# Optimization experiments

Measured on AMD Instinct MI355X. Metric: run time of the kernel, lower is better.

Reference implementation:

```python
import jax, jax.numpy as jnp
import numpy as np

B, C, L, K = 64, 2, 131072, 4


def setup_inputs() -> dict:
    key = jax.random.key(0)
    k1, k2, k3, k4 = jax.random.split(key, 4)
    x = jax.random.normal(k1, (B, C, L), dtype=jnp.float32)
    Bs = 0.5 * jax.random.normal(k2, (B, C, K, 3), dtype=jnp.float32)
    # Build stable denominators: complex-conjugate poles r*exp(+-j*theta), r < 0.95
    # a(z) = 1 - 2 r cos(theta) z^-1 + r^2 z^-2  -> guaranteed-stable IIR cascade.
    r = jax.random.uniform(k3, (B, C, K), minval=0.1, maxval=0.95)
    theta = jax.random.uniform(k4, (B, C, K), minval=0.05, maxval=np.pi - 0.05)
    a1 = -2.0 * r * jnp.cos(theta)
    a2 = r * r
    As = jnp.stack([jnp.ones_like(a1), a1, a2], axis=-1).astype(jnp.float32)
    return {"input_signal": x, "Bs": Bs, "As": As}


def _biquad_cascade(x, b, a):
    # x: [N, L]; b, a: [N, K, 3] with a already normalized (a0 == 1).
    # Serial cascade of K biquads, each in direct form II transposed:
    #   y[n]  = b0*u[n] + s1
    #   s1'   = b1*u[n] - a1*y[n] + s2
    #   s2'   = b2*u[n] - a2*y[n]
    # Exactly the linear recurrence the ssm/lfilter backends compute.
    nK = b.shape[1]
    b0, b1, b2 = b[..., 0], b[..., 1], b[..., 2]  # each [N, K]
    a1, a2 = a[..., 1], a[..., 2]

    def step(carry, xt):
        s1, s2 = carry  # each [N, K]
        u = xt  # [N]
        s1n, s2n = [], []
        for k in range(nK):  # small fixed cascade depth, unrolled
            y = b0[:, k] * u + s1[:, k]
            s1n.append(b1[:, k] * u - a1[:, k] * y + s2[:, k])
            s2n.append(b2[:, k] * u - a2[:, k] * y)
            u = y
        return (jnp.stack(s1n, axis=1), jnp.stack(s2n, axis=1)), u

    N = x.shape[0]
    init = (jnp.zeros((N, nK), x.dtype), jnp.zeros((N, nK), x.dtype))
    _, ys = jax.lax.scan(step, init, x.T)  # scan over time: ys [L, N]
    return ys.T


def reference(input_signal, Bs, As):
    b, c, audio_len = input_signal.shape
    assert Bs.shape[-1] == As.shape[-1] == 3
    # channel broadcasting as in _process_ssm
    if c == 1 and Bs.shape[1] > 1:
        input_signal = jnp.broadcast_to(input_signal, (b, Bs.shape[1], audio_len))
        c = Bs.shape[1]
    elif Bs.shape[1] == 1 and c > 1:
        Bs = jnp.broadcast_to(Bs, (b, c) + Bs.shape[2:])
        As = jnp.broadcast_to(As, (b, c) + As.shape[2:])
    a0 = As[..., :1]
    Bn = (Bs / a0).reshape(b * c, -1, 3)
    An = (As / a0).reshape(b * c, -1, 3)
    x = input_signal.reshape(b * c, audio_len)
    y = _biquad_cascade(x, Bn, An)
    return y.reshape(b, c, audio_len)
```

## Files before the change

kernel.cpp:

```cpp
#include <hip/hip_runtime.h>
#include <math.h>


#define SS   64
#define WMAX 384
#define WMIN 64
#define TT   32
#define TPB  256
#define LSTR 33
#define KB   4
#define NL   8
#define HALO 6
#define DSTR 9

typedef float vf4 __attribute__((ext_vector_type(4)));

__global__ void iir_prep2_kernel(const float* __restrict__ Bs,
                                 const float* __restrict__ As, int rows,
                                 int* __restrict__ nwrow,
                                 float* __restrict__ nmat)
{
    __shared__ float mat[4][3][64];
    const int grp  = threadIdx.x >> 6;
    const int lane = threadIdx.x & 63;
    const int row  = blockIdx.x * 4 + grp;
    const bool act = (row < rows);

    float b0[KB], b1[KB], b2[KB], na1[KB], na2[KB];
    if (act) {
        const float* Bp = Bs + (size_t)row * KB * 3;
        const float* Ap = As + (size_t)row * KB * 3;
#pragma unroll
        for (int k = 0; k < KB; ++k) {
            float inv = 1.0f / Ap[3 * k];
            b0[k]  =  Bp[3 * k]     * inv;
            b1[k]  =  Bp[3 * k + 1] * inv;
            b2[k]  =  Bp[3 * k + 2] * inv;
            na1[k] = -Ap[3 * k + 1] * inv;
            na2[k] = -Ap[3 * k + 2] * inv;
        }
    }

    float* cur = &mat[grp][0][0];
    float* nxt = &mat[grp][1][0];
    float* n1  = &mat[grp][2][0];

    if (act && lane < 8) {
        float s[8];
#pragma unroll
        for (int i = 0; i < 8; ++i) s[i] = (i == lane) ? 1.0f : 0.0f;
        float u = 0.0f;
#pragma unroll
        for (int k = 0; k < KB; ++k) {
            float y  = fmaf(b0[k], u, s[2 * k]);
            float t1 = fmaf(na1[k], y, fmaf(b1[k], u, s[2 * k + 1]));
            float t2 = fmaf(na2[k], y, b2[k] * u);
            s[2 * k] = t1; s[2 * k + 1] = t2; u = y;
        }
#pragma unroll
        for (int i = 0; i < 8; ++i) cur[i * 8 + lane] = s[i];
    }
    __syncthreads();

    const int i8 = lane >> 3, j8 = lane & 7;

    for (int t = 0; t < 6; ++t) {
        float acc = 0.0f;
        if (act) {
#pragma unroll
            for (int m = 0; m < 8; ++m)
                acc = fmaf(cur[i8 * 8 + m], cur[m * 8 + j8], acc);
            nxt[lane] = acc;
        }
        __syncthreads();
        float* t0 = cur; cur = nxt; nxt = t0;
    }

    if (act) {
        float v = cur[lane];
        n1[lane] = v;
        nmat[(size_t)row * 320 + lane] = v;
    }
    __syncthreads();

    for (int m = 2; m <= 5; ++m) {
        float acc = 0.0f;
        if (act) {
#pragma unroll
            for (int q = 0; q < 8; ++q)
                acc = fmaf(cur[i8 * 8 + q], n1[q * 8 + j8], acc);
            nxt[lane] = acc;
            nmat[(size_t)row * 320 + (m - 1) * 64 + lane] = acc;
        }
        __syncthreads();
        float* t0 = cur; cur = nxt; nxt = t0;
    }

    if (act && lane == 0) {
        const float* Ap = As + (size_t)row * KB * 3;
        float r2max = 0.0f;
#pragma unroll
        for (int k = 0; k < KB; ++k) {
            float a0 = Ap[3 * k];
            float a2 = Ap[3 * k + 2] / a0;
            r2max = fmaxf(r2max, a2);
        }
        float rmax = fminf(fmaxf(sqrtf(fmaxf(r2max, 0.f)), 0.20f), 0.955f);
        float Wf = 25.6f / (-logf(rmax));
        int W = ((int)ceilf(Wf) + TT - 1) & ~(TT - 1);
        W = min(max(W, WMIN), WMAX);
        nwrow[row] = (W + SS - 1) / SS;
    }
}

__global__ __launch_bounds__(TPB, 4) void iir_state_kernel(
    const float* __restrict__ x, const float* __restrict__ Bs,
    const float* __restrict__ As, int L, float* __restrict__ dstate)
{
    __shared__ float lds[TPB * LSTR];
    const int tid = threadIdx.x;
    const int cpr = L / SS;
    const int bpr = cpr / TPB;
    const int row = blockIdx.x / bpr;
    const int chunk0 = (blockIdx.x % bpr) * TPB;

    float b0[KB], b1[KB], b2[KB], na1[KB], na2[KB];
    const float* Bp = Bs + (size_t)row * KB * 3;
    const float* Ap = As + (size_t)row * KB * 3;
#pragma unroll
    for (int k = 0; k < KB; ++k) {
        float inv = 1.0f / Ap[3 * k];
        b0[k]  =  Bp[3 * k]     * inv;
        b1[k]  =  Bp[3 * k + 1] * inv;
        b2[k]  =  Bp[3 * k + 2] * inv;
        na1[k] = -Ap[3 * k + 1] * inv;
        na2[k] = -Ap[3 * k + 2] * inv;
    }

    float s1[KB] = {0.f, 0.f, 0.f, 0.f};
    float s2[KB] = {0.f, 0.f, 0.f, 0.f};

    const float* xrow = x + (size_t)row * L;
    float* myrow = lds + tid * LSTR;

    const int tq = tid >> 3;
    const int p4 = (tid & 7) << 2;
    int off[NL], ldsoff[NL];
#pragma unroll
    for (int l = 0; l < NL; ++l) {
        int j = l * 32 + tq;
        off[l]    = (chunk0 + j) * SS + p4;
        ldsoff[l] = j * LSTR + p4;
    }

    float4 rn[NL];
#pragma unroll
    for (int l = 0; l < NL; ++l)
        rn[l] = *reinterpret_cast<const float4*>(xrow + off[l]);

#pragma unroll
    for (int it = 0; it < SS / TT; ++it) {
        __syncthreads();
#pragma unroll
        for (int l = 0; l < NL; ++l) {
            float* d = lds + ldsoff[l];
            d[0] = rn[l].x; d[1] = rn[l].y; d[2] = rn[l].z; d[3] = rn[l].w;
        }
        if (it + 1 < SS / TT) {
            const int base = (it + 1) * TT;
#pragma unroll
            for (int l = 0; l < NL; ++l)
                rn[l] = *reinterpret_cast<const float4*>(xrow + off[l] + base);
        }
        __syncthreads();

#pragma unroll
        for (int p = 0; p < TT; ++p) {
            float u = myrow[p];
#pragma unroll
            for (int k = 0; k < KB; ++k) {
                float yv = fmaf(b0[k], u, s1[k]);
                s1[k] = fmaf(na1[k], yv, fmaf(b1[k], u, s2[k]));
                s2[k] = fmaf(na2[k], yv, b2[k] * u);
                u = yv;
            }
        }
    }

    float* dp = dstate + ((size_t)row * cpr + chunk0 + tid) * 8;
    float4 d0 = make_float4(s1[0], s2[0], s1[1], s2[1]);
    float4 d1 = make_float4(s1[2], s2[2], s1[3], s2[3]);
    *reinterpret_cast<float4*>(dp)     = d0;
    *reinterpret_cast<float4*>(dp + 4) = d1;
}

__global__ __launch_bounds__(TPB, 4) void iir_out_kernel(
    const float* __restrict__ x, const float* __restrict__ Bs,
    const float* __restrict__ As, float* __restrict__ out, int L,
    const float* __restrict__ dstate, const float* __restrict__ nmat,
    const int* __restrict__ nwrow)
{
    __shared__ float lds[TPB * LSTR];
    const int tid = threadIdx.x;
    const int cpr = L / SS;
    const int bpr = cpr / TPB;
    const int row = blockIdx.x / bpr;
    const int chunk0 = (blockIdx.x % bpr) * TPB;
    const int nW = nwrow[row];

    float b0[KB], b1[KB], b2[KB], na1[KB], na2[KB];
    const float* Bp = Bs + (size_t)row * KB * 3;
    const float* Ap = As + (size_t)row * KB * 3;
#pragma unroll
    for (int k = 0; k < KB; ++k) {
        float inv = 1.0f / Ap[3 * k];
        b0[k]  =  Bp[3 * k]     * inv;
        b1[k]  =  Bp[3 * k + 1] * inv;
        b2[k]  =  Bp[3 * k + 2] * inv;
        na1[k] = -Ap[3 * k + 1] * inv;
        na2[k] = -Ap[3 * k + 2] * inv;
    }

    const float* xrow = x   + (size_t)row * L;
    float*       orow = out + (size_t)row * L;
    float*       myrow = lds + tid * LSTR;

    const int tq = tid >> 3;
    const int p4 = (tid & 7) << 2;
    int off[NL], ldsoff[NL];
#pragma unroll
    for (int l = 0; l < NL; ++l) {
        int j = l * 32 + tq;
        off[l]    = (chunk0 + j) * SS + p4;
        ldsoff[l] = j * LSTR + p4;
    }

    float4 rn[NL];
#pragma unroll
    for (int l = 0; l < NL; ++l)
        rn[l] = *reinterpret_cast<const float4*>(xrow + off[l]);

    float* dl = lds;
    float* nl = lds + (TPB + HALO) * DSTR;
    const float* dbase = dstate + ((size_t)row * cpr + chunk0 - HALO) * 8;
    for (int e = tid; e < (TPB + HALO) * 8; e += TPB) {
        int c  = e >> 3;
        int gi = chunk0 - HALO + c;
        float v = 0.0f;
        if (gi >= 0) v = dbase[e];
        dl[c * DSTR + (e & 7)] = v;
    }
    for (int e = tid; e < 320; e += TPB) nl[e] = nmat[(size_t)row * 320 + e];
    __syncthreads();

    float p[8];
#pragma unroll
    for (int i = 0; i < 8; ++i) p[i] = dl[(tid + HALO - 1) * DSTR + i];
#pragma unroll 1
    for (int m = 2; m <= nW; ++m) {
        const float* M  = nl + (m - 2) * 64;
        const float* dd = dl + (tid + HALO - m) * DSTR;
        float din[8];
#pragma unroll
        for (int q = 0; q < 8; ++q) din[q] = dd[q];
#pragma unroll
        for (int i = 0; i < 8; ++i) {
            float a = p[i];
#pragma unroll
            for (int q = 0; q < 8; ++q) a = fmaf(M[i * 8 + q], din[q], a);
            p[i] = a;
        }
    }
    float s1[KB], s2[KB];
#pragma unroll
    for (int k = 0; k < KB; ++k) { s1[k] = p[2 * k]; s2[k] = p[2 * k + 1]; }

#pragma unroll
    for (int it = 0; it < SS / TT; ++it) {
        __syncthreads();
#pragma unroll
        for (int l = 0; l < NL; ++l) {
            float* d = lds + ldsoff[l];
            d[0] = rn[l].x; d[1] = rn[l].y; d[2] = rn[l].z; d[3] = rn[l].w;
        }
        if (it + 1 < SS / TT) {
            const int base = (it + 1) * TT;
#pragma unroll
            for (int l = 0; l < NL; ++l)
                rn[l] = *reinterpret_cast<const float4*>(xrow + off[l] + base);
        }
        __syncthreads();

#pragma unroll
        for (int q = 0; q < TT; ++q) {
            float u = myrow[q];
#pragma unroll
            for (int k = 0; k < KB; ++k) {
                float yv = fmaf(b0[k], u, s1[k]);
                s1[k] = fmaf(na1[k], yv, fmaf(b1[k], u, s2[k]));
                s2[k] = fmaf(na2[k], yv, b2[k] * u);
                u = yv;
            }
            myrow[q] = u;
        }
        __syncthreads();

        const int base = it * TT;
#pragma unroll
        for (int l = 0; l < NL; ++l) {
            const float* sp = lds + ldsoff[l];
            vf4 v = { sp[0], sp[1], sp[2], sp[3] };
            __builtin_nontemporal_store(
                v, reinterpret_cast<vf4*>(orow + off[l] + base));
        }
    }
}

__global__ void iir_prep_kernel(const float* __restrict__ As, int rows,
                                int* __restrict__ wrow, int* __restrict__ perm)
{
    __shared__ int sw[256];
    const int r = threadIdx.x;
    int W = 0;
    if (r < rows) {
        float r2max = 0.f;
#pragma unroll
        for (int k = 0; k < KB; ++k) {
            float a0 = As[(size_t)r * KB * 3 + 3 * k];
            float a2 = As[(size_t)r * KB * 3 + 3 * k + 2] / a0;
            r2max = fmaxf(r2max, a2);
        }
        float rmax = fminf(fmaxf(sqrtf(fmaxf(r2max, 0.f)), 0.20f), 0.955f);
        float Wf = 25.6f / (-logf(rmax));
        W = ((int)ceilf(Wf) + TT - 1) & ~(TT - 1);
        W = min(max(W, WMIN), WMAX);
        wrow[r] = W;
    }
    sw[r] = W;
    __syncthreads();
    if (r < rows) {
        int rank = 0;
        for (int i = 0; i < rows; ++i)
            rank += (sw[i] > W) || (sw[i] == W && i < r);
        perm[rank] = r;
    }
}

__global__ __launch_bounds__(TPB, 4) void iir_chunks_kernel(
    const float* __restrict__ x, const float* __restrict__ Bs,
    const float* __restrict__ As, float* __restrict__ out, int L,
    const int* __restrict__ wrow, const int* __restrict__ perm)
{
    __shared__ float lds[TPB * LSTR];
    const int tid = threadIdx.x;
    const int bpr = (L / SS) / TPB;
    const int row = perm[blockIdx.x / bpr];
    const int chunk0 = (blockIdx.x % bpr) * TPB;
    const int W = wrow[row];

    float b0[KB], b1[KB], b2[KB], na1[KB], na2[KB];
    const float* Bp = Bs + (size_t)row * KB * 3;
    const float* Ap = As + (size_t)row * KB * 3;
#pragma unroll
    for (int k = 0; k < KB; ++k) {
        float inv = 1.0f / Ap[3 * k];
        b0[k]  =  Bp[3 * k]     * inv;
        b1[k]  =  Bp[3 * k + 1] * inv;
        b2[k]  =  Bp[3 * k + 2] * inv;
        na1[k] = -Ap[3 * k + 1] * inv;
        na2[k] = -Ap[3 * k + 2] * inv;
    }

    float s1[KB] = {0.f, 0.f, 0.f, 0.f};
    float s2[KB] = {0.f, 0.f, 0.f, 0.f};

    const float* xrow = x   + (size_t)row * L;
    float*       orow = out + (size_t)row * L;
    float*       myrow = lds + tid * LSTR;

    const int tq = tid >> 3;
    const int p4 = (tid & 7) << 2;
    int off[NL], ldsoff[NL];
#pragma unroll
    for (int l = 0; l < NL; ++l) {
        int j = l * 32 + tq;
        off[l]    = (chunk0 + j) * SS + p4 - W;
        ldsoff[l] = j * LSTR + p4;
    }

    const int NT = (SS + W) / TT;
    const int WT = W / TT;

    float4 rn[NL];
#pragma unroll
    for (int l = 0; l < NL; ++l) {
        int pos = off[l];
        rn[l] = make_float4(0.f, 0.f, 0.f, 0.f);
        if (pos >= 0) rn[l] = *reinterpret_cast<const float4*>(xrow + pos);
    }

#pragma unroll 1
    for (int it = 0; it < NT; ++it) {
        __syncthreads();
#pragma unroll
        for (int l = 0; l < NL; ++l) {
            float* d = lds + ldsoff[l];
            d[0] = rn[l].x; d[1] = rn[l].y; d[2] = rn[l].z; d[3] = rn[l].w;
        }
        if (it + 1 < NT) {
            const int base = (it + 1) * TT;
#pragma unroll
            for (int l = 0; l < NL; ++l) {
                int pos = off[l] + base;
                rn[l] = make_float4(0.f, 0.f, 0.f, 0.f);
                if (pos >= 0) rn[l] = *reinterpret_cast<const float4*>(xrow + pos);
            }
        }
        __syncthreads();

        if (it < WT) {
#pragma unroll
            for (int p = 0; p < TT; ++p) {
                float u = myrow[p];
#pragma unroll
                for (int k = 0; k < KB; ++k) {
                    float yv = fmaf(b0[k], u, s1[k]);
                    s1[k] = fmaf(na1[k], yv, fmaf(b1[k], u, s2[k]));
                    s2[k] = fmaf(na2[k], yv, b2[k] * u);
                    u = yv;
                }
            }
        } else {
#pragma unroll
            for (int p = 0; p < TT; ++p) {
                float u = myrow[p];
#pragma unroll
                for (int k = 0; k < KB; ++k) {
                    float yv = fmaf(b0[k], u, s1[k]);
                    s1[k] = fmaf(na1[k], yv, fmaf(b1[k], u, s2[k]));
                    s2[k] = fmaf(na2[k], yv, b2[k] * u);
                    u = yv;
                }
                myrow[p] = u;
            }
            __syncthreads();

            const int base = it * TT - W;
#pragma unroll
            for (int l = 0; l < NL; ++l) {
                const float* sp = lds + ldsoff[l];
                vf4 v = { sp[0], sp[1], sp[2], sp[3] };
                __builtin_nontemporal_store(
                    v, reinterpret_cast<vf4*>(orow + off[l] + W + base));
            }
        }
    }
}

extern "C" void kernel_launch(void* const* d_in, const int* in_sizes, int n_in,
                              void* d_out, int out_size, void* d_ws, size_t ws_size,
                              hipStream_t stream) {
    const float* x  = (const float*)d_in[0];
    const float* Bs = (const float*)d_in[1];
    const float* As = (const float*)d_in[2];
    float* out = (float*)d_out;

    const int rows = in_sizes[1] / (KB * 3);
    const int L    = in_sizes[0] / rows;
    const int cpr  = L / SS;
    const int bpr  = cpr / TPB;

    float* dstate = (float*)d_ws;
    float* nmat   = dstate + (size_t)rows * cpr * 8;
    int*   nwrow  = (int*)(nmat + (size_t)rows * 320);
    const size_t need = (size_t)((char*)(nwrow + rows) - (char*)d_ws);

    if ((L % SS) == 0 && bpr * TPB == cpr && ws_size >= need) {
        hipLaunchKernelGGL(iir_prep2_kernel, dim3((rows + 3) / 4), dim3(256), 0,
                           stream, Bs, As, rows, nwrow, nmat);
        hipLaunchKernelGGL(iir_state_kernel, dim3(rows * bpr), dim3(TPB), 0,
                           stream, x, Bs, As, L, dstate);
        hipLaunchKernelGGL(iir_out_kernel, dim3(rows * bpr), dim3(TPB), 0,
                           stream, x, Bs, As, out, L, dstate, nmat, nwrow);
    } else {
        int* wrow = (int*)d_ws;
        int* perm = wrow + rows;
        hipLaunchKernelGGL(iir_prep_kernel, dim3(1), dim3(256), 0, stream,
                           As, rows, wrow, perm);
        hipLaunchKernelGGL(iir_chunks_kernel, dim3(rows * bpr), dim3(TPB), 0,
                           stream, x, Bs, As, out, L, wrow, perm);
    }
}
```

Before: 133.3 us.

## Fuse state and output passes into one cooperative kernel with grid sync

Replaces the separate state and output kernels with one cooperative kernel. Each thread runs its zero-state chunk once and keeps the outputs in registers. Only boundary halo states are exchanged across blocks through global memory and a grid-wide sync. The fused kernel then corrects the outputs using precomputed state-to-output matrices (wmat) built in the prep kernel. This removes the second read of x and the recomputation of the recurrence, but it needs the whole grid to be co-resident, adds a grid barrier, and raises register pressure by holding 64 outputs per thread. It falls back to the old two-kernel path when the grid cannot fit.

```diff
diff --git a/kernel.cpp b/kernel.cpp
--- a/kernel.cpp
+++ b/kernel.cpp
@@ -1,5 +1,8 @@
 #include <hip/hip_runtime.h>
+#include <hip/hip_cooperative_groups.h>
 #include <math.h>
+
+namespace cg = cooperative_groups;
 
 
 #define SS   64
@@ -18,9 +21,10 @@
 __global__ void iir_prep2_kernel(const float* __restrict__ Bs,
                                  const float* __restrict__ As, int rows,
                                  int* __restrict__ nwrow,
-                                 float* __restrict__ nmat)
+                                 float* __restrict__ nmat,
+                                 float* __restrict__ wmat)
 {
-    __shared__ float mat[4][3][64];
+    __shared__ float mat[4][5][64];
     const int grp  = threadIdx.x >> 6;
     const int lane = threadIdx.x & 63;
     const int row  = blockIdx.x * 4 + grp;
@@ -44,6 +48,8 @@
     float* cur = &mat[grp][0][0];
     float* nxt = &mat[grp][1][0];
     float* n1  = &mat[grp][2][0];
+    float* ac  = &mat[grp][3][0];
+    float* cw  = &mat[grp][4][0];
 
     if (act && lane < 8) {
         float s[8];
@@ -58,7 +64,8 @@
             s[2 * k] = t1; s[2 * k + 1] = t2; u = y;
         }
 #pragma unroll
-        for (int i = 0; i < 8; ++i) cur[i * 8 + lane] = s[i];
+        for (int i = 0; i < 8; ++i) { cur[i * 8 + lane] = s[i]; ac[i * 8 + lane] = s[i]; }
+        cw[lane] = u;
     }
     __syncthreads();
 
@@ -94,6 +101,23 @@
         }
         __syncthreads();
         float* t0 = cur; cur = nxt; nxt = t0;
+    }
+    __syncthreads();
+
+    if (act && lane < 8) {
+        float Ac[8];
+#pragma unroll
+        for (int i = 0; i < 8; ++i) Ac[i] = ac[i * 8 + lane];
+        float w = cw[lane];
+        float* wm = wmat + (size_t)row * 512;
+        for (int t = 0; t < SS; ++t) {
+            wm[t * 8 + lane] = w;
+            float acc = 0.0f;
+#pragma unroll
+            for (int i = 0; i < 8; ++i)
+                acc = fmaf(__shfl(w, i, 8), Ac[i], acc);
+            w = acc;
+        }
     }
 
     if (act && lane == 0) {
@@ -110,6 +134,162 @@
         int W = ((int)ceilf(Wf) + TT - 1) & ~(TT - 1);
         W = min(max(W, WMIN), WMAX);
         nwrow[row] = (W + SS - 1) / SS;
+    }
+}
+
+__global__ __launch_bounds__(TPB, 4) void iir_fused_kernel(
+    const float* __restrict__ x, const float* __restrict__ Bs,
+    const float* __restrict__ As, float* __restrict__ out, int L,
+    const float* __restrict__ nmat, const float* __restrict__ wmat,
+    const int* __restrict__ nwrow, float* __restrict__ halo)
+{
+    __shared__ float lds[TPB * LSTR];
+    const int tid = threadIdx.x;
+    const int cpr = L / SS;
+    const int bpr = cpr / TPB;
+    const int row = blockIdx.x / bpr;
+    const int blk = blockIdx.x % bpr;
+    const int chunk0 = blk * TPB;
+
+    float b0[KB], b1[KB], b2[KB], na1[KB], na2[KB];
+    const float* Bp = Bs + (size_t)row * KB * 3;
+    const float* Ap = As + (size_t)row * KB * 3;
+#pragma unroll
+    for (int k = 0; k < KB; ++k) {
+        float inv = 1.0f / Ap[3 * k];
+        b0[k]  =  Bp[3 * k]     * inv;
+        b1[k]  =  Bp[3 * k + 1] * inv;
+        b2[k]  =  Bp[3 * k + 2] * inv;
+        na1[k] = -Ap[3 * k + 1] * inv;
+        na2[k] = -Ap[3 * k + 2] * inv;
+    }
+
+    const float* xrow = x   + (size_t)row * L;
+    float*       orow = out + (size_t)row * L;
+    float*       myrow = lds + tid * LSTR;
+
+    const int tq = tid >> 3;
+    const int p4 = (tid & 7) << 2;
+    int off[NL], ldsoff[NL];
+#pragma unroll
+    for (int l = 0; l < NL; ++l) {
+        int j = l * 32 + tq;
+        off[l]    = (chunk0 + j) * SS + p4;
+        ldsoff[l] = j * LSTR + p4;
+    }
+
+    float y0[SS];
+    float s1[KB] = {0.f, 0.f, 0.f, 0.f};
+    float s2[KB] = {0.f, 0.f, 0.f, 0.f};
+
+    float4 rn[NL];
+#pragma unroll
+    for (int l = 0; l < NL; ++l)
+        rn[l] = *reinterpret_cast<const float4*>(xrow + off[l]);
+
+#pragma unroll
+    for (int it = 0; it < SS / TT; ++it) {
+        __syncthreads();
+#pragma unroll
+        for (int l = 0; l < NL; ++l) {
+            float* d = lds + ldsoff[l];
+            d[0] = rn[l].x; d[1] = rn[l].y; d[2] = rn[l].z; d[3] = rn[l].w;
+        }
+        if (it + 1 < SS / TT) {
+#pragma unroll
+            for (int l = 0; l < NL; ++l)
+                rn[l] = *reinterpret_cast<const float4*>(xrow + off[l] + (it + 1) * TT);
+        }
+        __syncthreads();
+
+#pragma unroll
+        for (int q = 0; q < TT; ++q) {
+            float u = myrow[q];
+#pragma unroll
+            for (int k = 0; k < KB; ++k) {
+                float yv = fmaf(b0[k], u, s1[k]);
+                s1[k] = fmaf(na1[k], yv, fmaf(b1[k], u, s2[k]));
+                s2[k] = fmaf(na2[k], yv, b2[k] * u);
+                u = yv;
+            }
+            y0[it * TT + q] = u;
+        }
+    }
+
+    __syncthreads();
+    float* dl = lds;
+#pragma unroll
+    for (int k = 0; k < KB; ++k) {
+        dl[(tid + HALO) * DSTR + 2 * k]     = s1[k];
+        dl[(tid + HALO) * DSTR + 2 * k + 1] = s2[k];
+    }
+    if (tid >= TPB - HALO) {
+        size_t hb = ((size_t)blockIdx.x * HALO + (tid - (TPB - HALO))) * 8;
+#pragma unroll
+        for (int k = 0; k < KB; ++k) {
+            __hip_atomic_store(&halo[hb + 2 * k],     s1[k], __ATOMIC_RELEASE, __HIP_MEMORY_SCOPE_AGENT);
+            __hip_atomic_store(&halo[hb + 2 * k + 1], s2[k], __ATOMIC_RELEASE, __HIP_MEMORY_SCOPE_AGENT);
+        }
+    }
+
+    cg::this_grid().sync();
+
+    if (tid < HALO) {
+        float v[8] = {0.f, 0.f, 0.f, 0.f, 0.f, 0.f, 0.f, 0.f};
+        if (blk > 0) {
+            size_t hb = ((size_t)(blockIdx.x - 1) * HALO + tid) * 8;
+#pragma unroll
+            for (int i = 0; i < 8; ++i)
+                v[i] = __hip_atomic_load(&halo[hb + i], __ATOMIC_ACQUIRE, __HIP_MEMORY_SCOPE_AGENT);
+        }
+#pragma unroll
+        for (int i = 0; i < 8; ++i) dl[tid * DSTR + i] = v[i];
+    }
+    __syncthreads();
+
+    const int nW = nwrow[row];
+    const float* Nrow = nmat + (size_t)row * 320;
+    const float* Wrow = wmat + (size_t)row * 512;
+    float pst[8];
+#pragma unroll
+    for (int i = 0; i < 8; ++i) pst[i] = dl[(tid + HALO - 1) * DSTR + i];
+#pragma unroll 1
+    for (int m = 2; m <= nW; ++m) {
+        const float* M  = Nrow + (m - 2) * 64;
+        const float* dd = dl + (tid + HALO - m) * DSTR;
+        float din[8];
+#pragma unroll
+        for (int q = 0; q < 8; ++q) din[q] = dd[q];
+#pragma unroll
+        for (int i = 0; i < 8; ++i) {
+            float a = pst[i];
+#pragma unroll
+            for (int q = 0; q < 8; ++q) a = fmaf(M[i * 8 + q], din[q], a);
+            pst[i] = a;
+        }
+    }
+
+#pragma unroll
+    for (int t = 0; t < SS; ++t) {
+        float a = y0[t];
+#pragma unroll
+        for (int i = 0; i < 8; ++i) a = fmaf(Wrow[t * 8 + i], pst[i], a);
+        y0[t] = a;
+    }
+
+#pragma unroll
+    for (int it = 0; it < SS / TT; ++it) {
+        __syncthreads();
+#pragma unroll
+        for (int q = 0; q < TT; ++q) myrow[q] = y0[it * TT + q];
+        __syncthreads();
+#pragma unroll
+        for (int l = 0; l < NL; ++l) {
+            const float* sp = lds + ldsoff[l];
+            vf4 v = { sp[0], sp[1], sp[2], sp[3] };
+            __builtin_nontemporal_store(
+                v, reinterpret_cast<vf4*>(orow + off[l] + it * TT));
+        }
     }
 }
 
@@ -469,19 +649,47 @@
     const int L    = in_sizes[0] / rows;
     const int cpr  = L / SS;
     const int bpr  = cpr / TPB;
+    const int grid = rows * bpr;
 
     float* dstate = (float*)d_ws;
-    float* nmat   = dstate + (size_t)rows * cpr * 8;
-    int*   nwrow  = (int*)(nmat + (size_t)rows * 320);
-    const size_t need = (size_t)((char*)(nwrow + rows) - (char*)d_ws);
-
-    if ((L % SS) == 0 && bpr * TPB == cpr && ws_size >= need) {
+    float* nmatp  = dstate + (size_t)rows * cpr * 8;
+    float* wmatp  = nmatp  + (size_t)rows * 320;
+    float* halop  = wmatp  + (size_t)rows * 512;
+    int*   nwrowp = (int*)(halop + (size_t)grid * HALO * 8);
+    const size_t need = (size_t)((char*)(nwrowp + rows) - (char*)d_ws);
+
+    const bool shape_ok = (L % SS) == 0 && bpr * TPB == cpr && ws_size >= need;
+
+    static int coopCap = -2;
+    if (coopCap == -2) {
+        int mb = 0, dev = 0, cus = 0;
+        if (hipOccupancyMaxActiveBlocksPerMultiprocessor(&mb, iir_fused_kernel,
+                                                         TPB, 0) != hipSuccess) mb = 0;
+        hipGetDevice(&dev);
+        if (hipDeviceGetAttribute(&cus, hipDeviceAttributeMultiprocessorCount,
+                                  dev) != hipSuccess) cus = 0;
+        coopCap = mb * cus;
+    }
+
+    if (shape_ok) {
         hipLaunchKernelGGL(iir_prep2_kernel, dim3((rows + 3) / 4), dim3(256), 0,
-                           stream, Bs, As, rows, nwrow, nmat);
-        hipLaunchKernelGGL(iir_state_kernel, dim3(rows * bpr), dim3(TPB), 0,
-                           stream, x, Bs, As, L, dstate);
-        hipLaunchKernelGGL(iir_out_kernel, dim3(rows * bpr), dim3(TPB), 0,
-                           stream, x, Bs, As, out, L, dstate, nmat, nwrow);
+                           stream, Bs, As, rows, nwrowp, nmatp, wmatp);
+        bool done = false;
+        if (coopCap >= grid) {
+            int Lv = L;
+            void* args[] = { (void*)&x, (void*)&Bs, (void*)&As, (void*)&out,
+                             (void*)&Lv, (void*)&nmatp, (void*)&wmatp,
+                             (void*)&nwrowp, (void*)&halop };
+            if (hipLaunchCooperativeKernel(iir_fused_kernel, dim3(grid), dim3(TPB),
+                                           args, 0, stream) == hipSuccess)
+                done = true;
+        }
+        if (!done) {
+            hipLaunchKernelGGL(iir_state_kernel, dim3(grid), dim3(TPB), 0,
+                               stream, x, Bs, As, L, dstate);
+            hipLaunchKernelGGL(iir_out_kernel, dim3(grid), dim3(TPB), 0,
+                               stream, x, Bs, As, out, L, dstate, nmatp, nwrowp);
+        }
     } else {
         int* wrow = (int*)d_ws;
         int* perm = wrow + rows;
```

Result: slower. 140.8 us (+5.7%).

## Write zero-state output in state pass and apply linear correction via precomputed response

Applied to the files above, without the earlier changes.

The state kernel now also writes the zero-initial-state filtered output to the output buffer. The output kernel becomes a correction kernel that reads that output back and adds the contribution of the chunk's true initial state, using a per-row 64x8 impulse-response table precomputed in the prep kernel. This replaces the serial biquad recurrence in the second pass with independent 8-term dot products, which removes the dependency chain. In exchange the output is written twice and read once more, so memory traffic rises, and the prep kernel gains a serial 64-step loop.

```diff
diff --git a/kernel.cpp b/kernel.cpp
--- a/kernel.cpp
+++ b/kernel.cpp
@@ -15,12 +15,13 @@
 
 typedef float vf4 __attribute__((ext_vector_type(4)));
 
-__global__ void iir_prep2_kernel(const float* __restrict__ Bs,
+__global__ void iir_prep3_kernel(const float* __restrict__ Bs,
                                  const float* __restrict__ As, int rows,
                                  int* __restrict__ nwrow,
-                                 float* __restrict__ nmat)
+                                 float* __restrict__ nmat,
+                                 float* __restrict__ wmat)
 {
-    __shared__ float mat[4][3][64];
+    __shared__ float mat[4][5][64];
     const int grp  = threadIdx.x >> 6;
     const int lane = threadIdx.x & 63;
     const int row  = blockIdx.x * 4 + grp;
@@ -44,6 +45,8 @@
     float* cur = &mat[grp][0][0];
     float* nxt = &mat[grp][1][0];
     float* n1  = &mat[grp][2][0];
+    float* ac  = &mat[grp][3][0];
+    float* cw  = &mat[grp][4][0];
 
     if (act && lane < 8) {
         float s[8];
@@ -58,7 +61,8 @@
             s[2 * k] = t1; s[2 * k + 1] = t2; u = y;
         }
 #pragma unroll
-        for (int i = 0; i < 8; ++i) cur[i * 8 + lane] = s[i];
+        for (int i = 0; i < 8; ++i) { cur[i * 8 + lane] = s[i]; ac[i * 8 + lane] = s[i]; }
+        cw[lane] = u;
     }
     __syncthreads();
 
@@ -94,6 +98,23 @@
         }
         __syncthreads();
         float* t0 = cur; cur = nxt; nxt = t0;
+    }
+    __syncthreads();
+
+    if (act && lane < 8) {
+        float Ac[8];
+#pragma unroll
+        for (int i = 0; i < 8; ++i) Ac[i] = ac[i * 8 + lane];
+        float w = cw[lane];
+        float* wm = wmat + (size_t)row * 512;
+        for (int t = 0; t < SS; ++t) {
+            wm[t * 8 + lane] = w;
+            float acc = 0.0f;
+#pragma unroll
+            for (int i = 0; i < 8; ++i)
+                acc = fmaf(__shfl(w, i, 8), Ac[i], acc);
+            w = acc;
+        }
     }
 
     if (act && lane == 0) {
@@ -113,9 +134,10 @@
     }
 }
 
-__global__ __launch_bounds__(TPB, 4) void iir_state_kernel(
+__global__ __launch_bounds__(TPB, 4) void iir_state_y0_kernel(
     const float* __restrict__ x, const float* __restrict__ Bs,
-    const float* __restrict__ As, int L, float* __restrict__ dstate)
+    const float* __restrict__ As, float* __restrict__ out, int L,
+    float* __restrict__ dstate)
 {
     __shared__ float lds[TPB * LSTR];
     const int tid = threadIdx.x;
@@ -140,8 +162,9 @@
     float s1[KB] = {0.f, 0.f, 0.f, 0.f};
     float s2[KB] = {0.f, 0.f, 0.f, 0.f};
 
-    const float* xrow = x + (size_t)row * L;
-    float* myrow = lds + tid * LSTR;
+    const float* xrow = x   + (size_t)row * L;
+    float*       orow = out + (size_t)row * L;
+    float*       myrow = lds + tid * LSTR;
 
     const int tq = tid >> 3;
     const int p4 = (tid & 7) << 2;
@@ -184,23 +207,31 @@
                 s2[k] = fmaf(na2[k], yv, b2[k] * u);
                 u = yv;
             }
+            myrow[p] = u;
+        }
+        __syncthreads();
+
+        const int base = it * TT;
+#pragma unroll
+        for (int l = 0; l < NL; ++l) {
+            const float* sp = lds + ldsoff[l];
+            float4 v = make_float4(sp[0], sp[1], sp[2], sp[3]);
+            *reinterpret_cast<float4*>(orow + off[l] + base) = v;
         }
     }
 
     float* dp = dstate + ((size_t)row * cpr + chunk0 + tid) * 8;
-    float4 d0 = make_float4(s1[0], s2[0], s1[1], s2[1]);
-    float4 d1 = make_float4(s1[2], s2[2], s1[3], s2[3]);
-    *reinterpret_cast<float4*>(dp)     = d0;
-    *reinterpret_cast<float4*>(dp + 4) = d1;
+    *reinterpret_cast<float4*>(dp)     = make_float4(s1[0], s2[0], s1[1], s2[1]);
+    *reinterpret_cast<float4*>(dp + 4) = make_float4(s1[2], s2[2], s1[3], s2[3]);
 }
 
-__global__ __launch_bounds__(TPB, 4) void iir_out_kernel(
-    const float* __restrict__ x, const float* __restrict__ Bs,
-    const float* __restrict__ As, float* __restrict__ out, int L,
+__global__ __launch_bounds__(TPB, 4) void iir_corr_kernel(
+    float* __restrict__ out, int L,
     const float* __restrict__ dstate, const float* __restrict__ nmat,
-    const int* __restrict__ nwrow)
+    const float* __restrict__ wmat, const int* __restrict__ nwrow)
 {
-    __shared__ float lds[TPB * LSTR];
+    __shared__ float lds[TPB * LSTR + 512];
+    float* wl = lds + TPB * LSTR;
     const int tid = threadIdx.x;
     const int cpr = L / SS;
     const int bpr = cpr / TPB;
@@ -208,22 +239,8 @@
     const int chunk0 = (blockIdx.x % bpr) * TPB;
     const int nW = nwrow[row];
 
-    float b0[KB], b1[KB], b2[KB], na1[KB], na2[KB];
-    const float* Bp = Bs + (size_t)row * KB * 3;
-    const float* Ap = As + (size_t)row * KB * 3;
-#pragma unroll
-    for (int k = 0; k < KB; ++k) {
-        float inv = 1.0f / Ap[3 * k];
-        b0[k]  =  Bp[3 * k]     * inv;
-        b1[k]  =  Bp[3 * k + 1] * inv;
-        b2[k]  =  Bp[3 * k + 2] * inv;
-        na1[k] = -Ap[3 * k + 1] * inv;
-        na2[k] = -Ap[3 * k + 2] * inv;
-    }
-
-    const float* xrow = x   + (size_t)row * L;
-    float*       orow = out + (size_t)row * L;
-    float*       myrow = lds + tid * LSTR;
+    float* orow  = out + (size_t)row * L;
+    float* myrow = lds + tid * LSTR;
 
     const int tq = tid >> 3;
     const int p4 = (tid & 7) << 2;
@@ -238,24 +255,25 @@
     float4 rn[NL];
 #pragma unroll
     for (int l = 0; l < NL; ++l)
-        rn[l] = *reinterpret_cast<const float4*>(xrow + off[l]);
+        rn[l] = *reinterpret_cast<const float4*>(orow + off[l]);
 
     float* dl = lds;
     float* nl = lds + (TPB + HALO) * DSTR;
-    const float* dbase = dstate + ((size_t)row * cpr + chunk0 - HALO) * 8;
+    const float* drow = dstate + (size_t)row * cpr * 8;
     for (int e = tid; e < (TPB + HALO) * 8; e += TPB) {
         int c  = e >> 3;
         int gi = chunk0 - HALO + c;
         float v = 0.0f;
-        if (gi >= 0) v = dbase[e];
+        if (gi >= 0) v = drow[(size_t)gi * 8 + (e & 7)];
         dl[c * DSTR + (e & 7)] = v;
     }
     for (int e = tid; e < 320; e += TPB) nl[e] = nmat[(size_t)row * 320 + e];
+    for (int e = tid; e < 512; e += TPB) wl[e] = wmat[(size_t)row * 512 + e];
     __syncthreads();
 
-    float p[8];
-#pragma unroll
-    for (int i = 0; i < 8; ++i) p[i] = dl[(tid + HALO - 1) * DSTR + i];
+    float pst[8];
+#pragma unroll
+    for (int i = 0; i < 8; ++i) pst[i] = dl[(tid + HALO - 1) * DSTR + i];
 #pragma unroll 1
     for (int m = 2; m <= nW; ++m) {
         const float* M  = nl + (m - 2) * 64;
@@ -265,15 +283,12 @@
         for (int q = 0; q < 8; ++q) din[q] = dd[q];
 #pragma unroll
         for (int i = 0; i < 8; ++i) {
-            float a = p[i];
+            float a = pst[i];
 #pragma unroll
             for (int q = 0; q < 8; ++q) a = fmaf(M[i * 8 + q], din[q], a);
-            p[i] = a;
-        }
-    }
-    float s1[KB], s2[KB];
-#pragma unroll
-    for (int k = 0; k < KB; ++k) { s1[k] = p[2 * k]; s2[k] = p[2 * k + 1]; }
+            pst[i] = a;
+        }
+    }
 
 #pragma unroll
     for (int it = 0; it < SS / TT; ++it) {
@@ -287,21 +302,18 @@
             const int base = (it + 1) * TT;
 #pragma unroll
             for (int l = 0; l < NL; ++l)
-                rn[l] = *reinterpret_cast<const float4*>(xrow + off[l] + base);
+                rn[l] = *reinterpret_cast<const float4*>(orow + off[l] + base);
         }
         __syncthreads();
 
 #pragma unroll
         for (int q = 0; q < TT; ++q) {
-            float u = myrow[q];
-#pragma unroll
-            for (int k = 0; k < KB; ++k) {
-                float yv = fmaf(b0[k], u, s1[k]);
-                s1[k] = fmaf(na1[k], yv, fmaf(b1[k], u, s2[k]));
-                s2[k] = fmaf(na2[k], yv, b2[k] * u);
-                u = yv;
-            }
-            myrow[q] = u;
+            const int t = it * TT + q;
+            float a = myrow[q];
+#pragma unroll
+            for (int i = 0; i < 8; ++i)
+                a = fmaf(wl[t * 8 + i], pst[i], a);
+            myrow[q] = a;
         }
         __syncthreads();
 
@@ -469,19 +481,21 @@
     const int L    = in_sizes[0] / rows;
     const int cpr  = L / SS;
     const int bpr  = cpr / TPB;
+    const int grid = rows * bpr;
 
     float* dstate = (float*)d_ws;
-    float* nmat   = dstate + (size_t)rows * cpr * 8;
-    int*   nwrow  = (int*)(nmat + (size_t)rows * 320);
-    const size_t need = (size_t)((char*)(nwrow + rows) - (char*)d_ws);
+    float* nmatp  = dstate + (size_t)rows * cpr * 8;
+    float* wmatp  = nmatp  + (size_t)rows * 320;
+    int*   nwrowp = (int*)(wmatp + (size_t)rows * 512);
+    const size_t need = (size_t)((char*)(nwrowp + rows) - (char*)d_ws);
 
     if ((L % SS) == 0 && bpr * TPB == cpr && ws_size >= need) {
-        hipLaunchKernelGGL(iir_prep2_kernel, dim3((rows + 3) / 4), dim3(256), 0,
-                           stream, Bs, As, rows, nwrow, nmat);
-        hipLaunchKernelGGL(iir_state_kernel, dim3(rows * bpr), dim3(TPB), 0,
-                           stream, x, Bs, As, L, dstate);
-        hipLaunchKernelGGL(iir_out_kernel, dim3(rows * bpr), dim3(TPB), 0,
-                           stream, x, Bs, As, out, L, dstate, nmat, nwrow);
+        hipLaunchKernelGGL(iir_prep3_kernel, dim3((rows + 3) / 4), dim3(256), 0,
+                           stream, Bs, As, rows, nwrowp, nmatp, wmatp);
+        hipLaunchKernelGGL(iir_state_y0_kernel, dim3(grid), dim3(TPB), 0,
+                           stream, x, Bs, As, out, L, dstate);
+        hipLaunchKernelGGL(iir_corr_kernel, dim3(grid), dim3(TPB), 0,
+                           stream, out, L, dstate, nmatp, wmatp, nwrowp);
     } else {
         int* wrow = (int*)d_ws;
         int* perm = wrow + rows;
```

New measurement: 155.2 us. 16.4% more time.
